# Performance work log

Hardware: AMD Instinct MI355X
Metric: run time of the kernel (lower is better)

The kernel has to match this reference:

```python
import jax, jax.numpy as jnp
import numpy as np

N_FEATURES = 4096
N_GROUPS = 1024
BATCH = 8192


def _make_groups():
    # Deterministic variable-size groups: size_g = 2 + (g % 7), sizes in [2, 8].
    rng = np.random.RandomState(0)
    sizes = 2 + (np.arange(N_GROUPS) % 7)
    flat_idx = rng.randint(0, N_FEATURES, size=int(sizes.sum())).astype(np.int64)
    seg_ids = np.repeat(np.arange(N_GROUPS, dtype=np.int64), sizes)
    return flat_idx, seg_ids


def setup_inputs() -> dict:
    key = jax.random.key(0)
    k1, k2, k3, k4 = jax.random.split(key, 4)
    flat_idx_np, seg_ids_np = _make_groups()
    total = flat_idx_np.shape[0]  # 5115
    x = jax.random.normal(k1, (BATCH, N_FEATURES), dtype=jnp.float32)
    # Concatenated per-group HeNormal-style weights (shape (size,1) flattened).
    w_flat = jax.random.normal(k2, (total,), dtype=jnp.float32)
    # SimplyConnected weight (Ones init in original; random here for testing).
    diag_w = jax.random.uniform(k3, (N_GROUPS,), dtype=jnp.float32)
    # Dense kernel [n_groups, units=1], no bias.
    dense_W = jax.random.normal(k4, (N_GROUPS, 1), dtype=jnp.float32) * (2.0 / N_GROUPS) ** 0.5
    return {
        "x": x,
        "flat_idx": jnp.asarray(flat_idx_np),
        "seg_ids": jnp.asarray(seg_ids_np),
        "w_flat": w_flat,
        "diag_w": diag_w,
        "dense_W": dense_W,
    }


def reference(x, flat_idx, seg_ids, w_flat, diag_w, dense_W):
    # GroupConnected: per-group gather + (size,1) matmul == segmented weighted sum.
    # gathered: [B, total_idx]; weighted then segment-summed over groups -> [B, n_groups]
    weighted = x[:, flat_idx] * w_flat  # [B, total]
    grouped = jax.ops.segment_sum(weighted.T, seg_ids, num_segments=N_GROUPS).T  # [B, G]
    # diagblock (depth-2 = 1 SimplyConnected): elementwise scale, then Dense (no bias).
    return (grouped * diag_w) @ dense_W  # [B, units=1]
```

## Files before the change

### kernel.cpp

```cpp
#include <hip/hip_runtime.h>

#define N_FEATURES 4096
#define N_GROUPS   1024
#define BATCH      8192

typedef float f32x4 __attribute__((ext_vector_type(4)));

__global__ __launch_bounds__(1024) void build_coeff_kernel(
    const int* __restrict__ flat_idx,
    const int* __restrict__ seg_ids,
    const float* __restrict__ w_flat,
    const float* __restrict__ diag_w,
    const float* __restrict__ dense_W,
    float* __restrict__ coeff,
    int total)
{
    __shared__ float s_coeff[N_FEATURES];
    for (int i = threadIdx.x; i < N_FEATURES; i += 1024) s_coeff[i] = 0.0f;
    __syncthreads();

#pragma unroll
    for (int k = 0; k < 5; ++k) {
        const int i = k * 1024 + (int)threadIdx.x;
        const bool valid = (i < total);
        const int  idx = valid ? flat_idx[i] : 0;
        const int  g   = valid ? seg_ids[i]  : 0;
        const float wv = valid ? w_flat[i]   : 0.0f;
        const float c  = wv * diag_w[g] * dense_W[g];
        if (valid) atomicAdd(&s_coeff[idx], c);
    }
    for (int i = 5 * 1024 + (int)threadIdx.x; i < total; i += 1024) {
        const int g = seg_ids[i];
        atomicAdd(&s_coeff[flat_idx[i]], w_flat[i] * diag_w[g] * dense_W[g]);
    }
    __syncthreads();
    for (int i = threadIdx.x; i < N_FEATURES; i += 1024) coeff[i] = s_coeff[i];
}

__global__ __launch_bounds__(256) void gemv_kernel(
    const float* __restrict__ x,
    const float* __restrict__ coeff,
    float* __restrict__ out)
{
    const int wid  = threadIdx.x >> 6;
    const int lane = threadIdx.x & 63;
    const int row  = (blockIdx.x << 2) | wid;

    const f32x4* __restrict__ xr = (const f32x4*)(x + (size_t)row * N_FEATURES);
    const f32x4* __restrict__ c4 = (const f32x4*)coeff;

    float acc = 0.0f;
#pragma unroll
    for (int k = 0; k < 16; ++k) {
        const int i = (k << 6) | lane;
        const f32x4 xv = __builtin_nontemporal_load(&xr[i]);
        const f32x4 cv = c4[i];
        acc += xv.x * cv.x + xv.y * cv.y + xv.z * cv.z + xv.w * cv.w;
    }

#pragma unroll
    for (int off = 32; off > 0; off >>= 1)
        acc += __shfl_down(acc, off, 64);

    if (lane == 0) out[row] = acc;
}

extern "C" void kernel_launch(void* const* d_in, const int* in_sizes, int n_in,
                              void* d_out, int out_size, void* d_ws, size_t ws_size,
                              hipStream_t stream) {
    const float* x        = (const float*)d_in[0];
    const int*   flat_idx = (const int*)d_in[1];
    const int*   seg_ids  = (const int*)d_in[2];
    const float* w_flat   = (const float*)d_in[3];
    const float* diag_w   = (const float*)d_in[4];
    const float* dense_W  = (const float*)d_in[5];
    float* out = (float*)d_out;
    const int total = in_sizes[1];

    float* coeff = (float*)d_ws;

    build_coeff_kernel<<<1, 1024, 0, stream>>>(flat_idx, seg_ids, w_flat,
                                               diag_w, dense_W, coeff, total);
    gemv_kernel<<<BATCH / 4, 256, 0, stream>>>(x, coeff, out);
}
```

Baseline: 196.7 us.

## Fuse coefficient build and GEMV into one cooperative kernel with grid sync

```diff
diff --git a/kernel.cpp b/kernel.cpp
--- a/kernel.cpp
+++ b/kernel.cpp
@@ -1,10 +1,106 @@
 #include <hip/hip_runtime.h>
+#include <hip/hip_cooperative_groups.h>
+
+namespace cg = cooperative_groups;
 
 #define N_FEATURES 4096
 #define N_GROUPS   1024
 #define BATCH      8192
 
 typedef float f32x4 __attribute__((ext_vector_type(4)));
+
+__global__ __launch_bounds__(256, 2) void fused_coop(
+    const float* __restrict__ x,
+    const int*   __restrict__ flat_idx,
+    const int*   __restrict__ seg_ids,
+    const float* __restrict__ w_flat,
+    const float* __restrict__ diag_w,
+    const float* __restrict__ dense_W,
+    float* __restrict__ coeff,
+    float* __restrict__ out,
+    int total)
+{
+    const int lane = threadIdx.x & 63;
+    const int wid  = threadIdx.x >> 6;
+    const int wave = (blockIdx.x << 2) | wid;
+    const int row0 = wave << 2;
+
+    __shared__ float s_coeff[N_FEATURES];
+    f32x4 a[16];
+    const bool builder = (blockIdx.x == 0);
+
+    if (builder) {
+        for (int i = threadIdx.x; i < N_FEATURES; i += 256) s_coeff[i] = 0.0f;
+        __syncthreads();
+#pragma unroll
+        for (int k = 0; k < 20; ++k) {
+            const int i = k * 256 + (int)threadIdx.x;
+            const bool valid = (i < total);
+            const int  idx = valid ? flat_idx[i] : 0;
+            const int  g   = valid ? seg_ids[i]  : 0;
+            const float wv = valid ? w_flat[i]   : 0.0f;
+            const float c  = wv * diag_w[g] * dense_W[g];
+            if (valid) atomicAdd(&s_coeff[idx], c);
+        }
+        for (int i = 20 * 256 + (int)threadIdx.x; i < total; i += 256) {
+            const int g = seg_ids[i];
+            atomicAdd(&s_coeff[flat_idx[i]], w_flat[i] * diag_w[g] * dense_W[g]);
+        }
+        __syncthreads();
+        for (int i = threadIdx.x; i < N_FEATURES; i += 256)
+            __hip_atomic_store(&coeff[i], s_coeff[i],
+                               __ATOMIC_RELAXED, __HIP_MEMORY_SCOPE_AGENT);
+    } else {
+        const f32x4* __restrict__ xr0 = (const f32x4*)(x + (size_t)row0 * N_FEATURES);
+#pragma unroll
+        for (int k = 0; k < 16; ++k)
+            a[k] = __builtin_nontemporal_load(&xr0[(k << 6) | lane]);
+    }
+
+    cg::this_grid().sync();
+
+    float c[64];
+    if (builder) {
+#pragma unroll
+        for (int k = 0; k < 16; ++k) {
+            const f32x4 cv = ((const f32x4*)s_coeff)[(k << 6) | lane];
+            c[4*k+0] = cv.x; c[4*k+1] = cv.y; c[4*k+2] = cv.z; c[4*k+3] = cv.w;
+        }
+    } else {
+#pragma unroll
+        for (int k = 0; k < 16; ++k) {
+            const int base = ((k << 6) | lane) << 2;
+#pragma unroll
+            for (int j = 0; j < 4; ++j)
+                c[4*k+j] = __hip_atomic_load(&coeff[base + j],
+                                             __ATOMIC_RELAXED, __HIP_MEMORY_SCOPE_AGENT);
+        }
+    }
+
+#pragma unroll
+    for (int r = 0; r < 4; ++r) {
+        const int row = row0 + r;
+        const f32x4* __restrict__ xr = (const f32x4*)(x + (size_t)row * N_FEATURES);
+        float acc = 0.0f;
+        if (r == 0 && !builder) {
+#pragma unroll
+            for (int k = 0; k < 16; ++k)
+                acc += a[k].x * c[4*k+0] + a[k].y * c[4*k+1]
+                     + a[k].z * c[4*k+2] + a[k].w * c[4*k+3];
+        } else {
+#pragma unroll
+            for (int k = 0; k < 16; ++k) {
+                const f32x4 xv = __builtin_nontemporal_load(&xr[(k << 6) | lane]);
+                acc += xv.x * c[4*k+0] + xv.y * c[4*k+1]
+                     + xv.z * c[4*k+2] + xv.w * c[4*k+3];
+            }
+        }
+#pragma unroll
+        for (int off = 32; off > 0; off >>= 1)
+            acc += __shfl_down(acc, off, 64);
+        if (lane == 0) out[row] = acc;
+    }
+}
 
 __global__ __launch_bounds__(1024) void build_coeff_kernel(
     const int* __restrict__ flat_idx,
@@ -18,7 +114,6 @@
     __shared__ float s_coeff[N_FEATURES];
     for (int i = threadIdx.x; i < N_FEATURES; i += 1024) s_coeff[i] = 0.0f;
     __syncthreads();
-
 #pragma unroll
     for (int k = 0; k < 5; ++k) {
         const int i = k * 1024 + (int)threadIdx.x;
@@ -57,11 +152,9 @@
         const f32x4 cv = c4[i];
         acc += xv.x * cv.x + xv.y * cv.y + xv.z * cv.z + xv.w * cv.w;
     }
-
 #pragma unroll
     for (int off = 32; off > 0; off >>= 1)
         acc += __shfl_down(acc, off, 64);
-
     if (lane == 0) out[row] = acc;
 }
 
@@ -74,12 +167,18 @@
     const float* w_flat   = (const float*)d_in[3];
     const float* diag_w   = (const float*)d_in[4];
     const float* dense_W  = (const float*)d_in[5];
-    float* out = (float*)d_out;
-    const int total = in_sizes[1];
+    float* out   = (float*)d_out;
+    float* coeff = (float*)d_ws;
+    int total = in_sizes[1];
 
-    float* coeff = (float*)d_ws;
-
-    build_coeff_kernel<<<1, 1024, 0, stream>>>(flat_idx, seg_ids, w_flat,
-                                               diag_w, dense_W, coeff, total);
-    gemv_kernel<<<BATCH / 4, 256, 0, stream>>>(x, coeff, out);
+    void* args[] = { (void*)&x, (void*)&flat_idx, (void*)&seg_ids, (void*)&w_flat,
+                     (void*)&diag_w, (void*)&dense_W, (void*)&coeff, (void*)&out,
+                     (void*)&total };
+    hipError_t err = hipLaunchCooperativeKernel((const void*)fused_coop,
+                                                dim3(512), dim3(256), args, 0, stream);
+    if (err != hipSuccess) {
+        build_coeff_kernel<<<1, 1024, 0, stream>>>(flat_idx, seg_ids, w_flat,
+                                                   diag_w, dense_W, coeff, total);
+        gemv_kernel<<<BATCH / 4, 256, 0, stream>>>(x, coeff, out);
+    }
 }
```

Result: slower. 285.3 us (+45.0%).
